# Performance work log

Measured on AMD Instinct MI355X. Metric: run time of the kernel, lower is better.

Reference implementation:

```python
import jax, jax.numpy as jnp
import numpy as np

B, C, D = 16384, 4096, 512
ALPHA = 0.1
BETA = 0.25


def setup_inputs() -> dict:
    key = jax.random.key(0)
    kx, kc = jax.random.split(key)
    x = jax.random.normal(kx, (B, D), dtype=jnp.float32)
    codes = jax.random.normal(kc, (1, C, D), dtype=jnp.float32)
    return {"x": x, "codes": codes}


def reference(x, codes):
    # x: (B, D), codes: (1, C, D). Eval-mode forward of Quantizer (l2 metric).
    d = x.shape[1]
    c = codes[0]                                  # (C, D)
    # squared l2 distance via expansion (same math as sum((x-c)^2, -1))
    x_sq = jnp.sum(x * x, axis=-1, keepdims=True)  # (B, 1)
    c_sq = jnp.sum(c * c, axis=-1)                 # (C,)
    dots = jnp.einsum('bd,cd->bc', x, c)           # (B, C)
    raw_distances = x_sq + c_sq[None, :] - 2.0 * dots
    distances = raw_distances / d / ALPHA          # scaling preserved for faithfulness
    indices = jnp.argmin(distances, axis=-1)       # (B,)
    quantized = c[indices]                         # (B, D) gather
    # commit loss: dist(x, stop_grad(quantized)); codebook loss: dist(stop_grad(x), quantized)
    diff_commit = x - jax.lax.stop_gradient(quantized)
    loss_commit = jnp.mean(jnp.sum(diff_commit * diff_commit, axis=-1))
    diff_code = jax.lax.stop_gradient(x) - quantized
    loss_codebook = jnp.mean(jnp.sum(diff_code * diff_code, axis=-1))
    loss = loss_commit + BETA * loss_codebook
    return quantized, indices, loss
```

## Files before the change

kernel.cpp:

```cpp
#include <hip/hip_runtime.h>

#define B_SZ 16384
#define C_SZ 4096
#define D_SZ 512

#define QSCALE 22.7f
#define INV_S2 (1.0f / (QSCALE * QSCALE))
#define EPS 6.0f
#define DBIAS 1024.0f

typedef __attribute__((ext_vector_type(4))) int intx4;

__device__ inline unsigned q4(const float4 v) {
    int a = (int)rintf(v.x * QSCALE); a = max(-127, min(127, a));
    int b = (int)rintf(v.y * QSCALE); b = max(-127, min(127, b));
    int c = (int)rintf(v.z * QSCALE); c = max(-127, min(127, c));
    int d = (int)rintf(v.w * QSCALE); d = max(-127, min(127, d));
    return ((unsigned)(a & 255)) | ((unsigned)(b & 255) << 8) |
           ((unsigned)(c & 255) << 16) | ((unsigned)(d & 255) << 24);
}
__device__ inline void gload16(const void* g, void* l) {
    __builtin_amdgcn_global_load_lds(
        (const __attribute__((address_space(1))) void*)g,
        (__attribute__((address_space(3))) void*)l, 16, 0, 0);
}

#define SCHEDB()  __builtin_amdgcn_sched_barrier(0)
#define VM0()     do { SCHEDB(); asm volatile("s_waitcnt vmcnt(0)"); SCHEDB(); } while (0)
#define LGKM0()   do { asm volatile("s_waitcnt lgkmcnt(0)"); SCHEDB(); } while (0)

#define ROR16(v, N) \
    ((unsigned)__builtin_amdgcn_update_dpp(0, (int)(v), 0x120 + (N), 0xF, 0xF, true))

__global__ __launch_bounds__(256) void convert_kernel(const float* __restrict__ x,
                                                      const float* __restrict__ codes,
                                                      unsigned* __restrict__ xq,
                                                      unsigned* __restrict__ cq,
                                                      float* __restrict__ csq) {
    const int XB = (B_SZ * D_SZ) / 4 / 256;
    if (blockIdx.x < XB) {
        const int tid = blockIdx.x * 256 + threadIdx.x;
        const float4 v = ((const float4*)x)[tid];
        xq[tid] = q4(v);
    } else {
        const int t = threadIdx.x;
        const int wave = t >> 6;
        const int lane = t & 63;
        const int code = (blockIdx.x - XB) * 4 + wave;
        const float4* cp = (const float4*)(codes + (size_t)code * D_SZ);
        float s = 0.0f;
        #pragma unroll
        for (int u = 0; u < 2; ++u) {
            const float4 v = cp[lane + 64 * u];
            cq[(size_t)code * (D_SZ / 4) + lane + 64 * u] = q4(v);
            s = fmaf(v.x, v.x, s); s = fmaf(v.y, v.y, s);
            s = fmaf(v.z, v.z, s); s = fmaf(v.w, v.w, s);
        }
        #pragma unroll
        for (int off = 32; off; off >>= 1) s += __shfl_down(s, off, 64);
        if (lane == 0) csq[code] = s;
    }
}

__global__ __launch_bounds__(512, 1) void gemm_argmin_kernel(
        const unsigned char* __restrict__ xq,
        const unsigned char* __restrict__ cq,
        const float* __restrict__ csq,
        uint2* __restrict__ table) {
    __shared__ unsigned char sB[4][256][128];
    __shared__ unsigned char sA[128][128];

    const int t = threadIdx.x;
    const int wave = t >> 6;
    const int lane = t & 63;
    const int quad = lane >> 4;
    const int l15 = lane & 15;
    const int wm = wave >> 2;
    const int wn = wave & 3;

    const int rowbase0 = blockIdx.y * 512;
    const int colbase = blockIdx.x * 256;

    const int lrow = lane >> 3;
    const int lchunk = (lane & 7) ^ lrow;
    const unsigned char* gA0 = xq + (size_t)(rowbase0 + wave * 16 + lrow) * D_SZ + lchunk * 16;
    const unsigned char* gB0 = cq + (size_t)(colbase + wave * 32 + lrow) * D_SZ + lchunk * 16;

    float cs2[4];
    #pragma unroll
    for (int j = 0; j < 4; ++j)
        cs2[j] = fmaf(0.5f, csq[colbase + wn * 64 + j * 16 + l15], DBIAS);

#define STAGE_A(rt, kt) do { \
        const unsigned char* _g = gA0 + (size_t)(rt) * 128 * D_SZ + (kt) * 128; \
        gload16(_g,                    &sA[wave * 16][0]); \
        gload16(_g + (size_t)8 * D_SZ, &sA[wave * 16 + 8][0]); \
    } while (0)
#define STAGE_B(kt) do { \
        const unsigned char* _g = gB0 + (kt) * 128; \
        _Pragma("unroll") for (int u = 0; u < 4; ++u) \
            gload16(_g + (size_t)(u * 8) * D_SZ, &sB[kt][wave * 32 + u * 8][0]); \
    } while (0)
#define LDA_REGS() do { \
        _Pragma("unroll") for (int ks = 0; ks < 2; ++ks) { \
            const int cc = (((ks * 4 + quad) ^ (l15 & 7))) * 16; \
            _Pragma("unroll") for (int i = 0; i < 4; ++i) \
                areg[ks][i] = *(const intx4*)&sA[wm * 64 + i * 16 + l15][cc]; \
        } \
    } while (0)
#define COMPUTE_KT(kt) do { \
        _Pragma("unroll") for (int ks = 0; ks < 2; ++ks) { \
            const int cc = (((ks * 4 + quad) ^ (l15 & 7))) * 16; \
            intx4 b[4]; \
            _Pragma("unroll") for (int j = 0; j < 4; ++j) \
                b[j] = *(const intx4*)&sB[kt][wn * 64 + j * 16 + l15][cc]; \
            _Pragma("unroll") for (int i = 0; i < 4; ++i) \
                _Pragma("unroll") for (int j = 0; j < 4; ++j) \
                    acc[i][j] = __builtin_amdgcn_mfma_i32_16x16x64_i8(areg[ks][i], b[j], acc[i][j], 0, 0, 0); \
        } \
    } while (0)
#define MERGE_STEP(N) do { \
        const unsigned ok1 = ROR16(k1, N); \
        const unsigned ok2 = ROR16(k2, N); \
        const unsigned hi = max(k1, ok1); \
        const unsigned w2 = (k1 < ok1) ? k2 : ok2; \
        k1 = min(k1, ok1); \
        k2 = min(hi, w2); \
    } while (0)

    STAGE_B(0);
    STAGE_A(0, 0);
    VM0();
    __syncthreads();

    const int hb = blockIdx.x * 4 + wn;

    for (int rt = 0; rt < 4; ++rt) {
        intx4 acc[4][4];
        #pragma unroll
        for (int i = 0; i < 4; ++i)
            #pragma unroll
            for (int j = 0; j < 4; ++j) acc[i][j] = (intx4)0;

        #pragma unroll
        for (int kt = 0; kt < 4; ++kt) {
            intx4 areg[2][4];
            LDA_REGS();
            LGKM0();
            __syncthreads();
            if (kt < 3) STAGE_A(rt, kt + 1);
            else if (rt < 3) STAGE_A(rt + 1, 0);
            if (rt == 0 && kt < 3) STAGE_B(kt + 1);
            COMPUTE_KT(kt);
            VM0();
            __syncthreads();
        }

        #pragma unroll
        for (int i = 0; i < 4; ++i) {
            #pragma unroll
            for (int r = 0; r < 4; ++r) {
                unsigned k[4];
                #pragma unroll
                for (int j = 0; j < 4; ++j) {
                    const float d = fmaf(-(float)acc[i][j][r], INV_S2, cs2[j]);
                    k[j] = (__float_as_uint(d) & 0xFFFFFFC0u) | (unsigned)(j * 16 + l15);
                }
                const unsigned lo1 = min(k[0], k[1]), hi1 = max(k[0], k[1]);
                const unsigned lo2 = min(k[2], k[3]), hi2 = max(k[2], k[3]);
                unsigned k1 = min(lo1, lo2);
                unsigned k2 = min(max(lo1, lo2), min(hi1, hi2));
                MERGE_STEP(8); MERGE_STEP(4); MERGE_STEP(2); MERGE_STEP(1);
                if (l15 == 0) {
                    const int grow = rowbase0 + rt * 128 + wm * 64 + i * 16 + quad * 4 + r;
                    table[(size_t)grow * 64 + hb] = make_uint2(k1, k2);
                }
            }
        }
    }
#undef STAGE_A
#undef STAGE_B
#undef LDA_REGS
#undef COMPUTE_KT
#undef MERGE_STEP
}

__global__ __launch_bounds__(256) void rerank_gather_loss_kernel(
        const float* __restrict__ x,
        const float* __restrict__ codes,
        const float* __restrict__ csq,
        const uint2* __restrict__ table,
        float* __restrict__ outq,
        float* __restrict__ out_idx_f,
        float* __restrict__ partials) {
    __shared__ float red[4];
    const int t = threadIdx.x;
    const int wave = t >> 6;
    const int lane = t & 63;
    const int row0 = (blockIdx.x * 4 + wave) * 4;

    uint2 e[4];
    float4 xv[4][2];
    #pragma unroll
    for (int r = 0; r < 4; ++r) {
        e[r] = table[(size_t)(row0 + r) * 64 + lane];
        const float4* xp = (const float4*)(x + (size_t)(row0 + r) * D_SZ);
        xv[r][0] = xp[lane];
        xv[r][1] = xp[lane + 64];
    }

    int fin[4];
    #pragma unroll
    for (int r = 0; r < 4; ++r) {
        const unsigned k1 = e[r].x, k2 = e[r].y;
        unsigned mk = k1;
        #pragma unroll
        for (int off = 32; off; off >>= 1)
            mk = min(mk, (unsigned)__shfl_xor((int)mk, off, 64));

        const float thr = __uint_as_float(mk & 0xFFFFFFC0u) + EPS;
        const float v1 = __uint_as_float(k1 & 0xFFFFFFC0u);
        const float v2 = __uint_as_float(k2 & 0xFFFFFFC0u);
        const unsigned long long b1 = __ballot(v1 <= thr);
        const unsigned long long b2 = __ballot(v2 <= thr);

        const unsigned long long bm = __ballot(k1 == mk);
        fin[r] = (__ffsll(bm) - 1) * 64 + (int)(mk & 63u);

        if (__popcll(b1) + __popcll(b2) > 1) {
            const int c1 = lane * 64 + (int)(k1 & 63u);
            const int c2 = lane * 64 + (int)(k2 & 63u);
            float bv = 3.4e38f; int bi = 0x7FFFFFFF;
            #pragma unroll
            for (int pass = 0; pass < 2; ++pass) {
                unsigned long long bb = pass ? b2 : b1;
                const int myc = pass ? c2 : c1;
                while (bb) {
                    const int src = __ffsll((unsigned long long)bb) - 1;
                    bb &= bb - 1;
                    const int ci = __shfl(myc, src, 64);
                    const float4* cp = (const float4*)(codes + (size_t)ci * D_SZ);
                    const float4 c0 = cp[lane];
                    const float4 c1v = cp[lane + 64];
                    float s = 0.0f;
                    s = fmaf(xv[r][0].x, c0.x, s);  s = fmaf(xv[r][0].y, c0.y, s);
                    s = fmaf(xv[r][0].z, c0.z, s);  s = fmaf(xv[r][0].w, c0.w, s);
                    s = fmaf(xv[r][1].x, c1v.x, s); s = fmaf(xv[r][1].y, c1v.y, s);
                    s = fmaf(xv[r][1].z, c1v.z, s); s = fmaf(xv[r][1].w, c1v.w, s);
                    #pragma unroll
                    for (int off = 32; off; off >>= 1) s += __shfl_xor(s, off, 64);
                    const float d = fmaf(0.5f, csq[ci], -s);
                    if (d < bv || (d == bv && ci < bi)) { bv = d; bi = ci; }
                }
            }
            fin[r] = bi;
        }
    }

    float4 qv[4][2];
    #pragma unroll
    for (int r = 0; r < 4; ++r) {
        const float4* qp = (const float4*)(codes + (size_t)fin[r] * D_SZ);
        qv[r][0] = qp[lane];
        qv[r][1] = qp[lane + 64];
    }

    float s = 0.0f;
    #pragma unroll
    for (int r = 0; r < 4; ++r) {
        float4* op = (float4*)(outq + (size_t)(row0 + r) * D_SZ);
        op[lane] = qv[r][0];
        op[lane + 64] = qv[r][1];
        const float d0 = xv[r][0].x - qv[r][0].x, d1 = xv[r][0].y - qv[r][0].y;
        const float d2 = xv[r][0].z - qv[r][0].z, d3 = xv[r][0].w - qv[r][0].w;
        const float d4 = xv[r][1].x - qv[r][1].x, d5 = xv[r][1].y - qv[r][1].y;
        const float d6 = xv[r][1].z - qv[r][1].z, d7 = xv[r][1].w - qv[r][1].w;
        s += d0 * d0 + d1 * d1 + d2 * d2 + d3 * d3 + d4 * d4 + d5 * d5 + d6 * d6 + d7 * d7;
        if (lane == 0) out_idx_f[row0 + r] = (float)fin[r];
    }
    #pragma unroll
    for (int off = 32; off; off >>= 1) s += __shfl_down(s, off, 64);
    if (lane == 0) red[wave] = s;
    __syncthreads();
    if (t == 0) partials[blockIdx.x] = red[0] + red[1] + red[2] + red[3];
}

__global__ __launch_bounds__(256) void loss_reduce_kernel(const float* __restrict__ partials,
                                                          float* __restrict__ loss_slot) {
    __shared__ float red[4];
    const int t = threadIdx.x;
    const int wave = t >> 6;
    const int lane = t & 63;
    float s = 0.0f;
    #pragma unroll
    for (int i = 0; i < (B_SZ / 16) / 256; ++i) s += partials[i * 256 + t];
    #pragma unroll
    for (int off = 32; off; off >>= 1) s += __shfl_down(s, off, 64);
    if (lane == 0) red[wave] = s;
    __syncthreads();
    if (t == 0)
        *loss_slot = (red[0] + red[1] + red[2] + red[3]) * (1.25f / (float)B_SZ);
}

extern "C" void kernel_launch(void* const* d_in, const int* in_sizes, int n_in,
                              void* d_out, int out_size, void* d_ws, size_t ws_size,
                              hipStream_t stream) {
    const float* x = (const float*)d_in[0];
    const float* codes = (const float*)d_in[1];

    float* outq = (float*)d_out;
    float* out_idx_f = outq + (size_t)B_SZ * D_SZ;
    float* loss_slot = out_idx_f + B_SZ;

    unsigned char* xq = (unsigned char*)d_ws;
    unsigned char* cq = xq + (size_t)B_SZ * D_SZ;
    float* csq = (float*)(cq + (size_t)C_SZ * D_SZ);
    uint2* table = (uint2*)(csq + C_SZ);
    float* partials = (float*)(table + (size_t)B_SZ * 64);

    const int XB = (B_SZ * D_SZ) / 4 / 256;
    const int CB = C_SZ / 4;
    convert_kernel<<<XB + CB, 256, 0, stream>>>(x, codes, (unsigned*)xq, (unsigned*)cq, csq);
    gemm_argmin_kernel<<<dim3(C_SZ / 256, B_SZ / 512), 512, 0, stream>>>(xq, cq, csq, table);
    rerank_gather_loss_kernel<<<B_SZ / 16, 256, 0, stream>>>(x, codes, csq, table, outq, out_idx_f, partials);
    loss_reduce_kernel<<<1, 256, 0, stream>>>(partials, loss_slot);
}
```

Measured before the change: 164.6 us.

## Load A fragments directly from global into registers, preload full B tile

Removes the LDS staging buffer for the quantized x tile. Each wave now reads its A fragments straight from global memory into registers, and the whole 256x512 codebook tile is loaded into LDS once before the loop. This drops the per-k-step barriers and the waitcnt synchronisation between loading and compute. In exchange, A loads are uncoalesced global reads that two wave-columns fetch redundantly, with no software prefetch, so MFMA may stall on global latency.

```diff
diff --git a/kernel.cpp b/kernel.cpp
--- a/kernel.cpp
+++ b/kernel.cpp
@@ -27,7 +27,6 @@
 
 #define SCHEDB()  __builtin_amdgcn_sched_barrier(0)
 #define VM0()     do { SCHEDB(); asm volatile("s_waitcnt vmcnt(0)"); SCHEDB(); } while (0)
-#define LGKM0()   do { asm volatile("s_waitcnt lgkmcnt(0)"); SCHEDB(); } while (0)
 
 #define ROR16(v, N) \
     ((unsigned)__builtin_amdgcn_update_dpp(0, (int)(v), 0x120 + (N), 0xF, 0xF, true))
@@ -68,7 +67,6 @@
         const float* __restrict__ csq,
         uint2* __restrict__ table) {
     __shared__ unsigned char sB[4][256][128];
-    __shared__ unsigned char sA[128][128];
 
     const int t = threadIdx.x;
     const int wave = t >> 6;
@@ -83,41 +81,19 @@
 
     const int lrow = lane >> 3;
     const int lchunk = (lane & 7) ^ lrow;
-    const unsigned char* gA0 = xq + (size_t)(rowbase0 + wave * 16 + lrow) * D_SZ + lchunk * 16;
     const unsigned char* gB0 = cq + (size_t)(colbase + wave * 32 + lrow) * D_SZ + lchunk * 16;
+
+    const unsigned char* gA0 = xq + (size_t)(rowbase0 + wm * 64 + l15) * D_SZ + quad * 16;
 
     float cs2[4];
     #pragma unroll
     for (int j = 0; j < 4; ++j)
         cs2[j] = fmaf(0.5f, csq[colbase + wn * 64 + j * 16 + l15], DBIAS);
 
-#define STAGE_A(rt, kt) do { \
-        const unsigned char* _g = gA0 + (size_t)(rt) * 128 * D_SZ + (kt) * 128; \
-        gload16(_g,                    &sA[wave * 16][0]); \
-        gload16(_g + (size_t)8 * D_SZ, &sA[wave * 16 + 8][0]); \
-    } while (0)
 #define STAGE_B(kt) do { \
         const unsigned char* _g = gB0 + (kt) * 128; \
         _Pragma("unroll") for (int u = 0; u < 4; ++u) \
             gload16(_g + (size_t)(u * 8) * D_SZ, &sB[kt][wave * 32 + u * 8][0]); \
-    } while (0)
-#define LDA_REGS() do { \
-        _Pragma("unroll") for (int ks = 0; ks < 2; ++ks) { \
-            const int cc = (((ks * 4 + quad) ^ (l15 & 7))) * 16; \
-            _Pragma("unroll") for (int i = 0; i < 4; ++i) \
-                areg[ks][i] = *(const intx4*)&sA[wm * 64 + i * 16 + l15][cc]; \
-        } \
-    } while (0)
-#define COMPUTE_KT(kt) do { \
-        _Pragma("unroll") for (int ks = 0; ks < 2; ++ks) { \
-            const int cc = (((ks * 4 + quad) ^ (l15 & 7))) * 16; \
-            intx4 b[4]; \
-            _Pragma("unroll") for (int j = 0; j < 4; ++j) \
-                b[j] = *(const intx4*)&sB[kt][wn * 64 + j * 16 + l15][cc]; \
-            _Pragma("unroll") for (int i = 0; i < 4; ++i) \
-                _Pragma("unroll") for (int j = 0; j < 4; ++j) \
-                    acc[i][j] = __builtin_amdgcn_mfma_i32_16x16x64_i8(areg[ks][i], b[j], acc[i][j], 0, 0, 0); \
-        } \
     } while (0)
 #define MERGE_STEP(N) do { \
         const unsigned ok1 = ROR16(k1, N); \
@@ -128,8 +104,7 @@
         k2 = min(hi, w2); \
     } while (0)
 
-    STAGE_B(0);
-    STAGE_A(0, 0);
+    STAGE_B(0); STAGE_B(1); STAGE_B(2); STAGE_B(3);
     VM0();
     __syncthreads();
 
@@ -142,18 +117,27 @@
             #pragma unroll
             for (int j = 0; j < 4; ++j) acc[i][j] = (intx4)0;
 
+        const unsigned char* gArt = gA0 + (size_t)rt * 128 * D_SZ;
+
         #pragma unroll
         for (int kt = 0; kt < 4; ++kt) {
-            intx4 areg[2][4];
-            LDA_REGS();
-            LGKM0();
-            __syncthreads();
-            if (kt < 3) STAGE_A(rt, kt + 1);
-            else if (rt < 3) STAGE_A(rt + 1, 0);
-            if (rt == 0 && kt < 3) STAGE_B(kt + 1);
-            COMPUTE_KT(kt);
-            VM0();
-            __syncthreads();
+            #pragma unroll
+            for (int ks = 0; ks < 2; ++ks) {
+                intx4 a[4];
+                #pragma unroll
+                for (int i = 0; i < 4; ++i)
+                    a[i] = *(const intx4*)(gArt + (size_t)(i * 16) * D_SZ + kt * 128 + ks * 64);
+                const int cc = (((ks * 4 + quad) ^ (l15 & 7))) * 16;
+                intx4 b[4];
+                #pragma unroll
+                for (int j = 0; j < 4; ++j)
+                    b[j] = *(const intx4*)&sB[kt][wn * 64 + j * 16 + l15][cc];
+                #pragma unroll
+                for (int i = 0; i < 4; ++i)
+                    #pragma unroll
+                    for (int j = 0; j < 4; ++j)
+                        acc[i][j] = __builtin_amdgcn_mfma_i32_16x16x64_i8(a[i], b[j], acc[i][j], 0, 0, 0);
+            }
         }
 
         #pragma unroll
@@ -178,10 +162,7 @@
             }
         }
     }
-#undef STAGE_A
 #undef STAGE_B
-#undef LDA_REGS
-#undef COMPUTE_KT
 #undef MERGE_STEP
 }
 
```

Result: slower. 189.7 us (+15.2%).
